# Kernel optimization log

Hardware: AMD Instinct MI355X
Metric: run time of the kernel (lower is better)

## Reference

```python
import jax, jax.numpy as jnp
import numpy as np

B, T, H, D = 4, 4096, 16, 64
BLOCK_SIZE = 64      # BS: local block size
NUM_GLOBAL = 64      # G: global tokens (first G positions)
NUM_RANDOM = 192     # R: random key positions shared by all blocks


def setup_inputs() -> dict:
    key = jax.random.key(0)
    kq, kk, kv, kr = jax.random.split(key, 4)
    q = jax.random.normal(kq, (B, T, H, D), dtype=jnp.float32)
    k = jax.random.normal(kk, (B, T, H, D), dtype=jnp.float32)
    v = jax.random.normal(kv, (B, T, H, D), dtype=jnp.float32)
    # torch.randperm(src_len)[:R] -> no duplicate indices
    rand_idx = jax.random.permutation(kr, T)[:NUM_RANDOM].astype(jnp.int32)
    return {"q": q, "k": k, "v": v, "rand_idx": rand_idx}


def _bigbird(q, k, v, rand_idx):
    Bq, Tq, Hq, Dq = q.shape
    inv_scale = Dq ** (-0.5)
    G, BS, R = NUM_GLOBAL, BLOCK_SIZE, NUM_RANDOM

    # --- global queries: full attention over all keys ---
    gs = jnp.einsum('bghd,bkhd->bhgk', q[:, :G], k) * inv_scale
    gw = jax.nn.softmax(gs, axis=-1)
    out_g = jnp.einsum('bhgk,bkhd->bghd', gw, v)  # (B, G, H, D)

    # --- non-global queries: local block + global + random keys, one softmax ---
    nb = (Tq - G) // BS  # (T - G) divisible by BS by construction
    qb = q[:, G:].reshape(Bq, nb, BS, Hq, Dq)
    kb = k[:, G:].reshape(Bq, nb, BS, Hq, Dq)
    vb = v[:, G:].reshape(Bq, nb, BS, Hq, Dq)
    kg, vg = k[:, :G], v[:, :G]            # (B, G, H, D)
    kr, vr = k[:, rand_idx], v[:, rand_idx]  # (B, R, H, D)

    s_loc = jnp.einsum('bnlhd,bnkhd->bnhlk', qb, kb)   # (B, nb, H, BS, BS)
    s_glo = jnp.einsum('bnlhd,bkhd->bnhlk', qb, kg)    # (B, nb, H, BS, G)
    s_rnd = jnp.einsum('bnlhd,bkhd->bnhlk', qb, kr)    # (B, nb, H, BS, R)
    s = jnp.concatenate([s_loc, s_glo, s_rnd], axis=-1) * inv_scale
    w = jax.nn.softmax(s, axis=-1)  # joint softmax over local|global|random keys
    w_loc, w_glo, w_rnd = w[..., :BS], w[..., BS:BS + G], w[..., BS + G:]

    out_b = (jnp.einsum('bnhlk,bnkhd->bnlhd', w_loc, vb)
             + jnp.einsum('bnhlk,bkhd->bnlhd', w_glo, vg)
             + jnp.einsum('bnhlk,bkhd->bnlhd', w_rnd, vr))
    out_b = out_b.reshape(Bq, Tq - G, Hq, Dq)

    return jnp.concatenate([out_g, out_b], axis=1)  # (B, T, H, D)


def reference(q, k, v, rand_idx):
    return _bigbird(q, k, v, rand_idx)
```

## Files before the change

kernel.cpp:

```cpp
#include <hip/hip_runtime.h>
#include <math.h>
#include <stdint.h>

#define BB 4
#define TT 4096
#define HH 16
#define DD 64
#define GG 64
#define NRND 192
#define HD 1024
#define NBH 64
#define QBLK 128
#define NSPQ 32
#define NCHUNK 4
#define SUBS (NCHUNK + NSPQ)

#define OFF_KBF  0ull
#define OFF_VT   33554432ull
#define OFF_KRT  67108864ull
#define OFF_VRT  68681728ull
#define OFF_WACC 70254592ull
#define OFF_WM   74448896ull
#define OFF_WL   74514432ull

typedef __attribute__((ext_vector_type(8))) short short8;
typedef __attribute__((ext_vector_type(16))) float f32x16;

__device__ __forceinline__ ushort rne_u(float f) {
    uint32_t u = __builtin_bit_cast(uint32_t, f);
    u += 0x7fffu + ((u >> 16) & 1u);
    return (ushort)(u >> 16);
}
__device__ __forceinline__ short bf_trunc_s(float f) {
    uint32_t u = __builtin_bit_cast(uint32_t, f);
    return (short)(u >> 16);
}
__device__ __forceinline__ float bf_back(short s) {
    uint32_t u = ((uint32_t)(uint16_t)s) << 16;
    return __builtin_bit_cast(float, u);
}
__device__ __forceinline__ float exp2_fast(float x) {
#if __has_builtin(__builtin_amdgcn_exp2f)
    return __builtin_amdgcn_exp2f(x);
#else
    float r; asm("v_exp_f32 %0, %1" : "=v"(r) : "v"(x)); return r;
#endif
}
__device__ __forceinline__ short8 ld8u(const ushort* p) {
    typedef __attribute__((ext_vector_type(4))) short short4v;
    short4v a = *(const short4v*)p;
    short4v b = *(const short4v*)(p + 4);
    short8 r;
    r[0]=a[0]; r[1]=a[1]; r[2]=a[2]; r[3]=a[3];
    r[4]=b[0]; r[5]=b[1]; r[6]=b[2]; r[7]=b[3];
    return r;
}

typedef const __attribute__((address_space(1))) uint32_t* gas1_t;
typedef __attribute__((address_space(3))) uint32_t* las3_t;
__device__ __forceinline__ void gld16(const void* g, void* l) {
    __builtin_amdgcn_global_load_lds((gas1_t)g, (las3_t)l, 16, 0, 0);
}

__global__ __launch_bounds__(256, 4)
void bb_prep(const float* __restrict__ K, const float* __restrict__ V,
             const int* __restrict__ RIDX, char* __restrict__ ws)
{
    __shared__ ushort tl[64][68];
    __shared__ int toks[NRND];
    const int bid = blockIdx.x, tid = threadIdx.x;
    const int r  = tid >> 2;
    const int d0 = (tid & 3) * 16;

    if (bid < 8192) {
        const bool isK = bid < 4096;
        const int id = isK ? bid : bid - 4096;
        const int bh = id >> 6, tile = id & 63;
        const int b = bh >> 4, h = bh & 15;
        const float* src = (isK ? K : V) + ((size_t)b*TT*HH + h)*DD
                         + (size_t)(tile*64 + r)*HD + d0;
        float f[16];
        #pragma unroll
        for (int i = 0; i < 16; i += 4) {
            const float4 v4 = *(const float4*)(src + i);
            f[i]=v4.x; f[i+1]=v4.y; f[i+2]=v4.z; f[i+3]=v4.w;
        }
        if (isK) {
            #pragma unroll
            for (int i = 0; i < 16; ++i) tl[r][d0+i] = rne_u(f[i]);
        } else {
            #pragma unroll
            for (int i = 0; i < 16; ++i) tl[d0+i][r] = rne_u(f[i]);
        }
        __syncthreads();
        char* obase = ws + (isK ? OFF_KBF : OFF_VT)
                    + (size_t)bh*524288 + (size_t)tile*8192;
        #pragma unroll
        for (int e = 0; e < 2; ++e) {
            const int uu = tid*2 + e;
            const int c = uu >> 6, rr = uu & 63;
            *(short8*)(obase + c*1024 + rr*16) = ld8u(&tl[rr][c*8]);
        }
    } else {
        const int bh = bid - 8192;
        const int b = bh >> 4, h = bh & 15;
        const size_t base = ((size_t)b*TT*HH + h)*DD;
        if (tid < NRND) toks[tid] = RIDX[tid];
        __syncthreads();
        for (int sub = 0; sub < 3; ++sub) {
            const int tok = toks[sub*64 + r];
            float f[16];
            const float* ks = K + base + (size_t)tok*HD + d0;
            #pragma unroll
            for (int i = 0; i < 16; i += 4) {
                const float4 v4 = *(const float4*)(ks + i);
                f[i]=v4.x; f[i+1]=v4.y; f[i+2]=v4.z; f[i+3]=v4.w;
            }
            #pragma unroll
            for (int i = 0; i < 16; ++i) tl[r][d0+i] = rne_u(f[i]);
            __syncthreads();
            {
                char* obase = ws + OFF_KRT + (size_t)bh*24576 + (size_t)sub*8192;
                #pragma unroll
                for (int e = 0; e < 2; ++e) {
                    const int uu = tid*2 + e;
                    const int c = uu >> 6, rr = uu & 63;
                    *(short8*)(obase + c*1024 + rr*16) = ld8u(&tl[rr][c*8]);
                }
            }
            __syncthreads();
            const float* vs = V + base + (size_t)tok*HD + d0;
            #pragma unroll
            for (int i = 0; i < 16; i += 4) {
                const float4 v4 = *(const float4*)(vs + i);
                f[i]=v4.x; f[i+1]=v4.y; f[i+2]=v4.z; f[i+3]=v4.w;
            }
            #pragma unroll
            for (int i = 0; i < 16; ++i) tl[d0+i][r] = rne_u(f[i]);
            __syncthreads();
            {
                char* obase = ws + OFF_VRT + (size_t)bh*24576 + (size_t)sub*8192;
                #pragma unroll
                for (int e = 0; e < 2; ++e) {
                    const int uu = tid*2 + e;
                    const int c = uu >> 6, rr = uu & 63;
                    *(short8*)(obase + c*1024 + rr*16) = ld8u(&tl[rr][c*8]);
                }
            }
            __syncthreads();
        }
    }
}

__global__ __launch_bounds__(512, 4)
void bb_mfma(const float* __restrict__ Q, float* __restrict__ OUT,
             char* __restrict__ ws)
{
    __shared__ __align__(16) char smem[34816];
    __shared__ float sm_m[2][QBLK];
    __shared__ float sm_l[2][QBLK];
    float (*osum)[67] = (float(*)[67])smem;

    const int tid  = threadIdx.x;
    const int lane = tid & 63;
    const int wid  = tid >> 6;
    const int wq   = wid >> 1;
    const int wk   = wid & 1;
    const int lq   = lane & 31;
    const int lh   = lane >> 5;

    const int j = blockIdx.x;
    const int r = j & 63;
    const int bh = ((r & 7) << 3) | (r >> 3);
    const int sub = j >> 6;
    const bool is_glob = sub < NCHUNK;
    int qtok0, ntiles, kt0 = 0, chunk = 0, tA = 0, tB = 0;
    if (is_glob) {
        chunk = sub; kt0 = chunk * 16; qtok0 = 0; ntiles = 16;
    } else {
        const int qi = sub - NCHUNK;
        qtok0 = GG + qi * QBLK;
        tA = 1 + 2 * qi;
        tB = (qi == 31) ? 63 : 2 + 2 * qi;
        ntiles = 6;
    }
    const int b  = bh >> 4;
    const int hd = bh & 15;
    const size_t bh_off = ((size_t)b * TT * HH + hd) * DD;

    const char* kbf_bh = ws + OFF_KBF + (size_t)bh * 524288;
    const char* vt_bh  = ws + OFF_VT  + (size_t)bh * 524288;
    const char* krt_bh = ws + OFF_KRT + (size_t)bh * 24576;
    const char* vrt_bh = ws + OFF_VRT + (size_t)bh * 24576;

    auto kbase = [&](int kt) -> const char* {
        if (is_glob) return kbf_bh + (size_t)(kt0 + kt) * 8192;
        if (kt == 0) return kbf_bh + (size_t)tA * 8192;
        if (kt == 1) return kbf_bh + (size_t)tB * 8192;
        if (kt == 2) return kbf_bh;
        return krt_bh + (size_t)(kt - 3) * 8192;
    };
    auto vbase = [&](int kt) -> const char* {
        if (is_glob) return vt_bh + (size_t)(kt0 + kt) * 8192;
        if (kt == 0) return vt_bh + (size_t)tA * 8192;
        if (kt == 1) return vt_bh + (size_t)tB * 8192;
        if (kt == 2) return vt_bh;
        return vrt_bh + (size_t)(kt - 3) * 8192;
    };

    const int qrow = wq * 32 + lq;
    int qoff;
    if (is_glob) qoff = qrow & 63;
    else         qoff = (qtok0 + qrow < TT) ? qrow : (qrow & 63);
    float4 qa[4], qb[4];
    {
        const float* qp = Q + bh_off + (size_t)(qtok0 + qoff) * HD;
        #pragma unroll
        for (int ks = 0; ks < 4; ++ks) {
            qa[ks] = *(const float4*)(qp + ks*16 + lh*8);
            qb[ks] = *(const float4*)(qp + ks*16 + lh*8 + 4);
        }
    }

    char* kbuf = smem;
    char* vbuf = smem + 16384;
    auto stage = [&](int buf, int kt_t) {
        const char* kb = kbase(kt_t);
        const char* vb = vbase(kt_t);
        gld16(kb + wid*1024 + lane*16, kbuf + buf*8192 + wid*1024);
        gld16(vb + wid*1024 + lane*16, vbuf + buf*8192 + wid*1024);
    };
    stage(0, 0);

    const float QSC = 0.18033688f;
    short8 qfh[4], qfl[4];
    #pragma unroll
    for (int ks = 0; ks < 4; ++ks) {
        float fv[8] = {qa[ks].x, qa[ks].y, qa[ks].z, qa[ks].w,
                       qb[ks].x, qb[ks].y, qb[ks].z, qb[ks].w};
        #pragma unroll
        for (int jj = 0; jj < 8; ++jj) {
            const float x = fv[jj] * QSC;
            const short hi = bf_trunc_s(x);
            qfh[ks][jj] = hi;
            qfl[ks][jj] = bf_trunc_s(x - bf_back(hi));
        }
    }

    f32x16 acc0, acc1;
    #pragma unroll
    for (int rr = 0; rr < 16; ++rr) { acc0[rr] = 0.f; acc1[rr] = 0.f; }
    float m_run = -INFINITY, l_run = 0.f;

    for (int kt = 0; kt < ntiles; ++kt) {
        const int cur = kt & 1;
        const bool hn = (kt + 1 < ntiles);
        if (hn) {
            stage(cur ^ 1, kt + 1);
            asm volatile("s_waitcnt vmcnt(2)" ::: "memory");
        } else {
            asm volatile("s_waitcnt vmcnt(0)" ::: "memory");
        }
        __builtin_amdgcn_s_barrier();
        asm volatile("" ::: "memory");

        const bool act = is_glob ? true
                       : (kt == 0) ? (wq < 2)
                       : (kt == 1) ? (wq >= 2) : true;
        if (act) {
            const char* kb = kbuf + cur*8192;
            const char* vb = vbuf + cur*8192;

            f32x16 sc;
            #pragma unroll
            for (int rr = 0; rr < 16; ++rr) sc[rr] = 0.f;
            {
                const int krow = wk*32 + lq;
                __builtin_amdgcn_s_setprio(1);
                #pragma unroll
                for (int ks = 0; ks < 4; ++ks) {
                    const short8 ak = *(const short8*)(kb + (ks*2 + lh)*1024 + krow*16);
                    sc = __builtin_amdgcn_mfma_f32_32x32x16_bf16(ak, qfh[ks], sc, 0, 0, 0);
                    sc = __builtin_amdgcn_mfma_f32_32x32x16_bf16(ak, qfl[ks], sc, 0, 0, 0);
                }
                __builtin_amdgcn_s_setprio(0);
            }

            float pm = sc[0];
            #pragma unroll
            for (int rr = 1; rr < 16; ++rr) pm = fmaxf(pm, sc[rr]);
            pm = fmaxf(pm, __shfl_xor(pm, 32));
            if (__any(pm > m_run + 11.5f)) {
                const float mnew = fmaxf(m_run, pm);
                const float cf = exp2_fast(m_run - mnew);
                l_run *= cf;
                #pragma unroll
                for (int rr = 0; rr < 16; ++rr) { acc0[rr] *= cf; acc1[rr] *= cf; }
                m_run = mnew;
            }
            float ls = 0.f;
            #pragma unroll
            for (int rr = 0; rr < 16; ++rr) {
                sc[rr] = exp2_fast(sc[rr] - m_run);
                ls += sc[rr];
            }
            ls += __shfl_xor(ls, 32);
            l_run += ls;

            #pragma unroll
            for (int s = 0; s < 2; ++s) {
                uint32_t a01, a23, a45, a67;
                asm("v_cvt_pk_bf16_f32 %0, %1, %2" : "=v"(a01) : "v"(sc[8*s+0]), "v"(sc[8*s+1]));
                asm("v_cvt_pk_bf16_f32 %0, %1, %2" : "=v"(a23) : "v"(sc[8*s+2]), "v"(sc[8*s+3]));
                asm("v_cvt_pk_bf16_f32 %0, %1, %2" : "=v"(a45) : "v"(sc[8*s+4]), "v"(sc[8*s+5]));
                asm("v_cvt_pk_bf16_f32 %0, %1, %2" : "=v"(a67) : "v"(sc[8*s+6]), "v"(sc[8*s+7]));
                asm("v_permlane32_swap_b32 %0, %1" : "+v"(a01), "+v"(a45));
                asm("v_permlane32_swap_b32 %0, %1" : "+v"(a23), "+v"(a67));
                union { uint32_t u[4]; short8 v; } pfu;
                pfu.u[0] = a01; pfu.u[1] = a23; pfu.u[2] = a45; pfu.u[3] = a67;
                const int cb = wk*4 + s*2 + lh;
                const short8 v0 = *(const short8*)(vb + cb*1024 + lq*16);
                const short8 v1 = *(const short8*)(vb + cb*1024 + (lq + 32)*16);
                __builtin_amdgcn_s_setprio(1);
                acc0 = __builtin_amdgcn_mfma_f32_32x32x16_bf16(v0, pfu.v, acc0, 0, 0, 0);
                acc1 = __builtin_amdgcn_mfma_f32_32x32x16_bf16(v1, pfu.v, acc1, 0, 0, 0);
                __builtin_amdgcn_s_setprio(0);
            }
        }

        if (hn) {
            asm volatile("" ::: "memory");
            __builtin_amdgcn_s_barrier();
            asm volatile("" ::: "memory");
        }
    }

    if (lane < 32) { sm_m[wk][qrow] = m_run; sm_l[wk][qrow] = l_run; }
    __syncthreads();
    const float Mq  = fmaxf(sm_m[0][qrow], sm_m[1][qrow]);
    const float wsc = exp2_fast(m_run - Mq);
    if (wk == 0) {
        #pragma unroll
        for (int rr = 0; rr < 16; ++rr) {
            const int dr = (rr & 3) + 8*(rr >> 2) + 4*lh;
            osum[qrow][dr     ] = acc0[rr] * wsc;
            osum[qrow][dr + 32] = acc1[rr] * wsc;
        }
    }
    __syncthreads();
    if (wk == 1) {
        #pragma unroll
        for (int rr = 0; rr < 16; ++rr) {
            const int dr = (rr & 3) + 8*(rr >> 2) + 4*lh;
            osum[qrow][dr     ] += acc0[rr] * wsc;
            osum[qrow][dr + 32] += acc1[rr] * wsc;
        }
    }
    __syncthreads();
    {
        const int q  = tid >> 2;
        const int d0 = (tid & 3) * 16;
        const float M     = fmaxf(sm_m[0][q], sm_m[1][q]);
        const float lcomb = exp2_fast(sm_m[0][q] - M) * sm_l[0][q]
                          + exp2_fast(sm_m[1][q] - M) * sm_l[1][q];
        if (is_glob) {
            if (q < 64) {
                float* WACC = (float*)(ws + OFF_WACC);
                float* WM   = (float*)(ws + OFF_WM);
                float* WL   = (float*)(ws + OFF_WL);
                const int slot = chunk * NBH + bh;
                float* dst = WACC + (size_t)slot * 4096 + q * 64 + d0;
                #pragma unroll
                for (int i = 0; i < 16; i += 4) {
                    float4 o;
                    o.x = osum[q][d0 + i    ];
                    o.y = osum[q][d0 + i + 1];
                    o.z = osum[q][d0 + i + 2];
                    o.w = osum[q][d0 + i + 3];
                    *(float4*)(dst + i) = o;
                }
                if ((tid & 3) == 0) {
                    WM[slot * 64 + q] = M;
                    WL[slot * 64 + q] = lcomb;
                }
            }
        } else if (qtok0 + q < TT) {
            const float inv = 1.f / lcomb;
            float* dst = OUT + bh_off + (size_t)(qtok0 + q) * HD + d0;
            #pragma unroll
            for (int i = 0; i < 16; i += 4) {
                float4 o;
                o.x = osum[q][d0 + i    ] * inv;
                o.y = osum[q][d0 + i + 1] * inv;
                o.z = osum[q][d0 + i + 2] * inv;
                o.w = osum[q][d0 + i + 3] * inv;
                *(float4*)(dst + i) = o;
            }
        }
    }
}

__global__ __launch_bounds__(256, 4)
void bb_combine(const char* __restrict__ ws, float* __restrict__ OUT)
{
    const int bh = blockIdx.x;
    const int b  = bh >> 4;
    const int hd = bh & 15;
    const size_t bh_off = ((size_t)b * TT * HH + hd) * DD;

    const float* WACC = (const float*)(ws + OFF_WACC);
    const float* WM   = (const float*)(ws + OFF_WM);
    const float* WL   = (const float*)(ws + OFF_WL);

    const int q  = threadIdx.x >> 2;
    const int d0 = (threadIdx.x & 3) * 16;

    float m[NCHUNK];
    float M = -INFINITY;
    #pragma unroll
    for (int c = 0; c < NCHUNK; ++c) {
        m[c] = WM[(c * NBH + bh) * 64 + q];
        M = fmaxf(M, m[c]);
    }
    float w[NCHUNK];
    float denom = 0.f;
    #pragma unroll
    for (int c = 0; c < NCHUNK; ++c) {
        w[c] = exp2_fast(m[c] - M);
        denom += w[c] * WL[(c * NBH + bh) * 64 + q];
    }
    const float inv = 1.f / denom;

    float* dst = OUT + bh_off + (size_t)q * HD + d0;
    #pragma unroll
    for (int i = 0; i < 16; i += 4) {
        float ox = 0.f, oy = 0.f, oz = 0.f, ow = 0.f;
        #pragma unroll
        for (int c = 0; c < NCHUNK; ++c) {
            const float4 a = *(const float4*)&WACC[(size_t)(c * NBH + bh) * 4096 + q * 64 + d0 + i];
            ox += w[c] * a.x; oy += w[c] * a.y;
            oz += w[c] * a.z; ow += w[c] * a.w;
        }
        float4 o; o.x = ox * inv; o.y = oy * inv; o.z = oz * inv; o.w = ow * inv;
        *(float4*)(dst + i) = o;
    }
}

extern "C" void kernel_launch(void* const* d_in, const int* in_sizes, int n_in,
                              void* d_out, int out_size, void* d_ws, size_t ws_size,
                              hipStream_t stream) {
    const float* Q    = (const float*)d_in[0];
    const float* K    = (const float*)d_in[1];
    const float* V    = (const float*)d_in[2];
    const int*   RIDX = (const int*)d_in[3];
    float* OUT = (float*)d_out;
    char*  ws  = (char*)d_ws;

    hipLaunchKernelGGL(bb_prep, dim3(8192 + 64), dim3(256), 0, stream,
                       K, V, RIDX, ws);
    hipLaunchKernelGGL(bb_mfma, dim3(NBH * SUBS), dim3(512), 0, stream,
                       Q, OUT, ws);
    hipLaunchKernelGGL(bb_combine, dim3(NBH), dim3(256), 0, stream, ws, OUT);
}
```

Before: 132.3 us.

## Drop LDS staging, read K/V fragments straight from global with register prefetch

The main attention kernel no longer stages K/V tiles into shared memory via global_load_lds with double buffering and barriers. Each 256-thread block now handles 64 queries instead of 128, and each wave loads its K and V MFMA fragments directly from global memory, prefetching the next tile's K into registers while computing the current one. Removing barriers and the half-idle waves on local tiles is meant to cut sync overhead and wasted work. In exchange, neighbouring waves fetch the same K/V data redundantly from L2, and the grid grows to more, smaller blocks.

Result: slower. 187.0 us (+41.4%).

```diff
diff --git a/kernel.cpp b/kernel.cpp
--- a/kernel.cpp
+++ b/kernel.cpp
@@ -10,10 +10,9 @@
 #define NRND 192
 #define HD 1024
 #define NBH 64
-#define QBLK 128
-#define NSPQ 32
 #define NCHUNK 4
-#define SUBS (NCHUNK + NSPQ)
+#define NGBLK (NBH*NCHUNK)
+#define NSPB  (NBH*63)
 
 #define OFF_KBF  0ull
 #define OFF_VT   33554432ull
@@ -54,12 +53,6 @@
     r[0]=a[0]; r[1]=a[1]; r[2]=a[2]; r[3]=a[3];
     r[4]=b[0]; r[5]=b[1]; r[6]=b[2]; r[7]=b[3];
     return r;
-}
-
-typedef const __attribute__((address_space(1))) uint32_t* gas1_t;
-typedef __attribute__((address_space(3))) uint32_t* las3_t;
-__device__ __forceinline__ void gld16(const void* g, void* l) {
-    __builtin_amdgcn_global_load_lds((gas1_t)g, (las3_t)l, 16, 0, 0);
 }
 
 __global__ __launch_bounds__(256, 4)
@@ -152,14 +145,13 @@
     }
 }
 
-__global__ __launch_bounds__(512, 4)
+__global__ __launch_bounds__(256, 4)
 void bb_mfma(const float* __restrict__ Q, float* __restrict__ OUT,
              char* __restrict__ ws)
 {
-    __shared__ __align__(16) char smem[34816];
-    __shared__ float sm_m[2][QBLK];
-    __shared__ float sm_l[2][QBLK];
-    float (*osum)[67] = (float(*)[67])smem;
+    __shared__ float osum[64][67];
+    __shared__ float sm_m[2][64];
+    __shared__ float sm_l[2][64];
 
     const int tid  = threadIdx.x;
     const int lane = tid & 63;
@@ -168,21 +160,22 @@
     const int wk   = wid & 1;
     const int lq   = lane & 31;
     const int lh   = lane >> 5;
+    const int krow = wk*32 + lq;
+    const int cb0  = (wk*4 + lh) * 1024;
+    const int cb1  = (wk*4 + 2 + lh) * 1024;
 
     const int j = blockIdx.x;
-    const int r = j & 63;
-    const int bh = ((r & 7) << 3) | (r >> 3);
-    const int sub = j >> 6;
-    const bool is_glob = sub < NCHUNK;
-    int qtok0, ntiles, kt0 = 0, chunk = 0, tA = 0, tB = 0;
+    const bool is_glob = j < NGBLK;
+    int bh, qtok0, chunk = 0, kt0 = 0;
     if (is_glob) {
-        chunk = sub; kt0 = chunk * 16; qtok0 = 0; ntiles = 16;
+        chunk = j >> 6;
+        bh    = (j & 7) + 8 * ((j >> 3) & 7);
+        kt0   = chunk * 16;
+        qtok0 = 0;
     } else {
-        const int qi = sub - NCHUNK;
-        qtok0 = GG + qi * QBLK;
-        tA = 1 + 2 * qi;
-        tB = (qi == 31) ? 63 : 2 + 2 * qi;
-        ntiles = 6;
+        const int js = j - NGBLK;
+        bh    = (js & 7) + 8 * ((js >> 3) & 7);
+        qtok0 = GG + (js >> 6) * 64;
     }
     const int b  = bh >> 4;
     const int hd = bh & 15;
@@ -193,44 +186,15 @@
     const char* krt_bh = ws + OFF_KRT + (size_t)bh * 24576;
     const char* vrt_bh = ws + OFF_VRT + (size_t)bh * 24576;
 
-    auto kbase = [&](int kt) -> const char* {
-        if (is_glob) return kbf_bh + (size_t)(kt0 + kt) * 8192;
-        if (kt == 0) return kbf_bh + (size_t)tA * 8192;
-        if (kt == 1) return kbf_bh + (size_t)tB * 8192;
-        if (kt == 2) return kbf_bh;
-        return krt_bh + (size_t)(kt - 3) * 8192;
-    };
-    auto vbase = [&](int kt) -> const char* {
-        if (is_glob) return vt_bh + (size_t)(kt0 + kt) * 8192;
-        if (kt == 0) return vt_bh + (size_t)tA * 8192;
-        if (kt == 1) return vt_bh + (size_t)tB * 8192;
-        if (kt == 2) return vt_bh;
-        return vrt_bh + (size_t)(kt - 3) * 8192;
-    };
-
-    const int qrow = wq * 32 + lq;
-    int qoff;
-    if (is_glob) qoff = qrow & 63;
-    else         qoff = (qtok0 + qrow < TT) ? qrow : (qrow & 63);
     float4 qa[4], qb[4];
     {
-        const float* qp = Q + bh_off + (size_t)(qtok0 + qoff) * HD;
+        const float* qp = Q + bh_off + (size_t)(qtok0 + wq*32 + lq) * HD;
         #pragma unroll
         for (int ks = 0; ks < 4; ++ks) {
             qa[ks] = *(const float4*)(qp + ks*16 + lh*8);
             qb[ks] = *(const float4*)(qp + ks*16 + lh*8 + 4);
         }
     }
-
-    char* kbuf = smem;
-    char* vbuf = smem + 16384;
-    auto stage = [&](int buf, int kt_t) {
-        const char* kb = kbase(kt_t);
-        const char* vb = vbase(kt_t);
-        gld16(kb + wid*1024 + lane*16, kbuf + buf*8192 + wid*1024);
-        gld16(vb + wid*1024 + lane*16, vbuf + buf*8192 + wid*1024);
-    };
-    stage(0, 0);
 
     const float QSC = 0.18033688f;
     short8 qfh[4], qfl[4];
@@ -252,89 +216,96 @@
     for (int rr = 0; rr < 16; ++rr) { acc0[rr] = 0.f; acc1[rr] = 0.f; }
     float m_run = -INFINITY, l_run = 0.f;
 
-    for (int kt = 0; kt < ntiles; ++kt) {
-        const int cur = kt & 1;
-        const bool hn = (kt + 1 < ntiles);
-        if (hn) {
-            stage(cur ^ 1, kt + 1);
-            asm volatile("s_waitcnt vmcnt(2)" ::: "memory");
-        } else {
-            asm volatile("s_waitcnt vmcnt(0)" ::: "memory");
-        }
-        __builtin_amdgcn_s_barrier();
-        asm volatile("" ::: "memory");
-
-        const bool act = is_glob ? true
-                       : (kt == 0) ? (wq < 2)
-                       : (kt == 1) ? (wq >= 2) : true;
-        if (act) {
-            const char* kb = kbuf + cur*8192;
-            const char* vb = vbuf + cur*8192;
-
-            f32x16 sc;
-            #pragma unroll
-            for (int rr = 0; rr < 16; ++rr) sc[rr] = 0.f;
-            {
-                const int krow = wk*32 + lq;
-                __builtin_amdgcn_s_setprio(1);
-                #pragma unroll
-                for (int ks = 0; ks < 4; ++ks) {
-                    const short8 ak = *(const short8*)(kb + (ks*2 + lh)*1024 + krow*16);
-                    sc = __builtin_amdgcn_mfma_f32_32x32x16_bf16(ak, qfh[ks], sc, 0, 0, 0);
-                    sc = __builtin_amdgcn_mfma_f32_32x32x16_bf16(ak, qfl[ks], sc, 0, 0, 0);
-                }
-                __builtin_amdgcn_s_setprio(0);
-            }
-
-            float pm = sc[0];
-            #pragma unroll
-            for (int rr = 1; rr < 16; ++rr) pm = fmaxf(pm, sc[rr]);
-            pm = fmaxf(pm, __shfl_xor(pm, 32));
-            if (__any(pm > m_run + 11.5f)) {
-                const float mnew = fmaxf(m_run, pm);
-                const float cf = exp2_fast(m_run - mnew);
-                l_run *= cf;
-                #pragma unroll
-                for (int rr = 0; rr < 16; ++rr) { acc0[rr] *= cf; acc1[rr] *= cf; }
-                m_run = mnew;
-            }
-            float ls = 0.f;
-            #pragma unroll
-            for (int rr = 0; rr < 16; ++rr) {
-                sc[rr] = exp2_fast(sc[rr] - m_run);
-                ls += sc[rr];
-            }
-            ls += __shfl_xor(ls, 32);
-            l_run += ls;
-
-            #pragma unroll
-            for (int s = 0; s < 2; ++s) {
-                uint32_t a01, a23, a45, a67;
-                asm("v_cvt_pk_bf16_f32 %0, %1, %2" : "=v"(a01) : "v"(sc[8*s+0]), "v"(sc[8*s+1]));
-                asm("v_cvt_pk_bf16_f32 %0, %1, %2" : "=v"(a23) : "v"(sc[8*s+2]), "v"(sc[8*s+3]));
-                asm("v_cvt_pk_bf16_f32 %0, %1, %2" : "=v"(a45) : "v"(sc[8*s+4]), "v"(sc[8*s+5]));
-                asm("v_cvt_pk_bf16_f32 %0, %1, %2" : "=v"(a67) : "v"(sc[8*s+6]), "v"(sc[8*s+7]));
-                asm("v_permlane32_swap_b32 %0, %1" : "+v"(a01), "+v"(a45));
-                asm("v_permlane32_swap_b32 %0, %1" : "+v"(a23), "+v"(a67));
-                union { uint32_t u[4]; short8 v; } pfu;
-                pfu.u[0] = a01; pfu.u[1] = a23; pfu.u[2] = a45; pfu.u[3] = a67;
-                const int cb = wk*4 + s*2 + lh;
-                const short8 v0 = *(const short8*)(vb + cb*1024 + lq*16);
-                const short8 v1 = *(const short8*)(vb + cb*1024 + (lq + 32)*16);
-                __builtin_amdgcn_s_setprio(1);
-                acc0 = __builtin_amdgcn_mfma_f32_32x32x16_bf16(v0, pfu.v, acc0, 0, 0, 0);
-                acc1 = __builtin_amdgcn_mfma_f32_32x32x16_bf16(v1, pfu.v, acc1, 0, 0, 0);
-                __builtin_amdgcn_s_setprio(0);
-            }
-        }
-
-        if (hn) {
-            asm volatile("" ::: "memory");
-            __builtin_amdgcn_s_barrier();
-            asm volatile("" ::: "memory");
-        }
-    }
-
+    auto ldK = [&](const char* kb, short8 (&kf)[4]) {
+        #pragma unroll
+        for (int ks = 0; ks < 4; ++ks)
+            kf[ks] = *(const short8*)(kb + (ks*2 + lh)*1024 + krow*16);
+    };
+
+    auto tile = [&](const char* vb, const char* kbn,
+                    short8 (&kc)[4], short8 (&kn)[4], bool pf) {
+        short8 vf0, vf1, vf2, vf3;
+        vf0 = *(const short8*)(vb + cb0 + lq*16);
+        vf1 = *(const short8*)(vb + cb0 + (lq + 32)*16);
+        vf2 = *(const short8*)(vb + cb1 + lq*16);
+        vf3 = *(const short8*)(vb + cb1 + (lq + 32)*16);
+        if (pf) ldK(kbn, kn);
+
+        f32x16 sc;
+        #pragma unroll
+        for (int rr = 0; rr < 16; ++rr) sc[rr] = 0.f;
+        __builtin_amdgcn_s_setprio(1);
+        #pragma unroll
+        for (int ks = 0; ks < 4; ++ks) {
+            sc = __builtin_amdgcn_mfma_f32_32x32x16_bf16(kc[ks], qfh[ks], sc, 0, 0, 0);
+            sc = __builtin_amdgcn_mfma_f32_32x32x16_bf16(kc[ks], qfl[ks], sc, 0, 0, 0);
+        }
+        __builtin_amdgcn_s_setprio(0);
+
+        float pm = sc[0];
+        #pragma unroll
+        for (int rr = 1; rr < 16; ++rr) pm = fmaxf(pm, sc[rr]);
+        pm = fmaxf(pm, __shfl_xor(pm, 32));
+        if (__any(pm > m_run + 11.5f)) {
+            const float mnew = fmaxf(m_run, pm);
+            const float cf = exp2_fast(m_run - mnew);
+            l_run *= cf;
+            #pragma unroll
+            for (int rr = 0; rr < 16; ++rr) { acc0[rr] *= cf; acc1[rr] *= cf; }
+            m_run = mnew;
+        }
+        float ls = 0.f;
+        #pragma unroll
+        for (int rr = 0; rr < 16; ++rr) {
+            sc[rr] = exp2_fast(sc[rr] - m_run);
+            ls += sc[rr];
+        }
+        ls += __shfl_xor(ls, 32);
+        l_run += ls;
+
+        #pragma unroll
+        for (int s = 0; s < 2; ++s) {
+            uint32_t a01, a23, a45, a67;
+            asm("v_cvt_pk_bf16_f32 %0, %1, %2" : "=v"(a01) : "v"(sc[8*s+0]), "v"(sc[8*s+1]));
+            asm("v_cvt_pk_bf16_f32 %0, %1, %2" : "=v"(a23) : "v"(sc[8*s+2]), "v"(sc[8*s+3]));
+            asm("v_cvt_pk_bf16_f32 %0, %1, %2" : "=v"(a45) : "v"(sc[8*s+4]), "v"(sc[8*s+5]));
+            asm("v_cvt_pk_bf16_f32 %0, %1, %2" : "=v"(a67) : "v"(sc[8*s+6]), "v"(sc[8*s+7]));
+            asm("v_permlane32_swap_b32 %0, %1" : "+v"(a01), "+v"(a45));
+            asm("v_permlane32_swap_b32 %0, %1" : "+v"(a23), "+v"(a67));
+            union { uint32_t u[4]; short8 v; } pfu;
+            pfu.u[0] = a01; pfu.u[1] = a23; pfu.u[2] = a45; pfu.u[3] = a67;
+            const short8 va = (s == 0) ? vf0 : vf2;
+            const short8 vbb = (s == 0) ? vf1 : vf3;
+            __builtin_amdgcn_s_setprio(1);
+            acc0 = __builtin_amdgcn_mfma_f32_32x32x16_bf16(va,  pfu.v, acc0, 0, 0, 0);
+            acc1 = __builtin_amdgcn_mfma_f32_32x32x16_bf16(vbb, pfu.v, acc1, 0, 0, 0);
+            __builtin_amdgcn_s_setprio(0);
+        }
+    };
+
+    short8 kA[4], kB[4];
+    if (is_glob) {
+        const char* kb = kbf_bh + (size_t)kt0 * 8192;
+        const char* vb = vt_bh  + (size_t)kt0 * 8192;
+        ldK(kb, kA);
+        #pragma unroll 1
+        for (int it = 0; it < 8; ++it) {
+            tile(vb,        kb + 8192,  kA, kB, true);
+            tile(vb + 8192, kb + 16384, kB, kA, it < 7);
+            kb += 16384; vb += 16384;
+        }
+    } else {
+        const char* kbL = kbf_bh + (size_t)(qtok0 >> 6) * 8192;
+        const char* vbL = vt_bh  + (size_t)(qtok0 >> 6) * 8192;
+        ldK(kbL, kA);
+        tile(vbL,              kbf_bh,           kA, kB, true);
+        tile(vt_bh,            krt_bh,           kB, kA, true);
+        tile(vrt_bh,           krt_bh + 8192,    kA, kB, true);
+        tile(vrt_bh + 8192,    krt_bh + 16384,   kB, kA, true);
+        tile(vrt_bh + 16384,   krt_bh,           kA, kB, false);
+    }
+
+    const int qrow = wq*32 + lq;
     if (lane < 32) { sm_m[wk][qrow] = m_run; sm_l[wk][qrow] = l_run; }
     __syncthreads();
     const float Mq  = fmaxf(sm_m[0][qrow], sm_m[1][qrow]);
@@ -364,27 +335,25 @@
         const float lcomb = exp2_fast(sm_m[0][q] - M) * sm_l[0][q]
                           + exp2_fast(sm_m[1][q] - M) * sm_l[1][q];
         if (is_glob) {
-            if (q < 64) {
-                float* WACC = (float*)(ws + OFF_WACC);
-                float* WM   = (float*)(ws + OFF_WM);
-                float* WL   = (float*)(ws + OFF_WL);
-                const int slot = chunk * NBH + bh;
-                float* dst = WACC + (size_t)slot * 4096 + q * 64 + d0;
-                #pragma unroll
-                for (int i = 0; i < 16; i += 4) {
-                    float4 o;
-                    o.x = osum[q][d0 + i    ];
-                    o.y = osum[q][d0 + i + 1];
-                    o.z = osum[q][d0 + i + 2];
-                    o.w = osum[q][d0 + i + 3];
-                    *(float4*)(dst + i) = o;
-                }
-                if ((tid & 3) == 0) {
-                    WM[slot * 64 + q] = M;
-                    WL[slot * 64 + q] = lcomb;
-                }
-            }
-        } else if (qtok0 + q < TT) {
+            float* WACC = (float*)(ws + OFF_WACC);
+            float* WM   = (float*)(ws + OFF_WM);
+            float* WL   = (float*)(ws + OFF_WL);
+            const int slot = chunk * NBH + bh;
+            float* dst = WACC + (size_t)slot * 4096 + q * 64 + d0;
+            #pragma unroll
+            for (int i = 0; i < 16; i += 4) {
+                float4 o;
+                o.x = osum[q][d0 + i    ];
+                o.y = osum[q][d0 + i + 1];
+                o.z = osum[q][d0 + i + 2];
+                o.w = osum[q][d0 + i + 3];
+                *(float4*)(dst + i) = o;
+            }
+            if ((tid & 3) == 0) {
+                WM[slot * 64 + q] = M;
+                WL[slot * 64 + q] = lcomb;
+            }
+        } else {
             const float inv = 1.f / lcomb;
             float* dst = OUT + bh_off + (size_t)(qtok0 + q) * HD + d0;
             #pragma unroll
@@ -458,7 +427,7 @@
 
     hipLaunchKernelGGL(bb_prep, dim3(8192 + 64), dim3(256), 0, stream,
                        K, V, RIDX, ws);
-    hipLaunchKernelGGL(bb_mfma, dim3(NBH * SUBS), dim3(512), 0, stream,
+    hipLaunchKernelGGL(bb_mfma, dim3(NGBLK + NSPB), dim3(256), 0, stream,
                        Q, OUT, ws);
     hipLaunchKernelGGL(bb_combine, dim3(NBH), dim3(256), 0, stream, ws, OUT);
 }
```
